# Kernel optimization log

Measured on AMD Instinct MI355X. Metric: run time of the kernel, lower is better.

The kernel has to match this reference:

```python
import jax, jax.numpy as jnp
import numpy as np

NUM_EXPERTS = 64
TOP_K = 2
TEMPERATURE = 1.0
MOMENTUM = 0.9


def _l2norm(x, axis=-1):
    # torch F.normalize: x / max(||x||, eps)
    n = jnp.linalg.norm(x, axis=axis, keepdims=True)
    return x / jnp.maximum(n, 1e-12)


def setup_inputs() -> dict:
    key = jax.random.key(0)
    k1, k2 = jax.random.split(key)
    hidden_states = jax.random.normal(k1, (4, 4096, 2048), dtype=jnp.float32)
    centers = _l2norm(jax.random.normal(k2, (NUM_EXPERTS, 2048), dtype=jnp.float32))
    return {"hidden_states": hidden_states, "centers": centers}


def reference(hidden_states, centers):
    B, T, H = hidden_states.shape
    flat = hidden_states.reshape(-1, H).astype(jnp.float32)  # [N, H]
    N = flat.shape[0]

    # cosine-similarity logits
    reps_n = _l2norm(flat)
    centers_n = _l2norm(centers)
    temp = jnp.maximum(jnp.float32(TEMPERATURE), 1e-6)
    logits = (reps_n @ centers_n.T) / temp  # [N, E]

    probs = jax.nn.softmax(logits, axis=-1)
    top_w, top_ids = jax.lax.top_k(probs, TOP_K)  # [N, k]
    top_w = top_w / (jnp.sum(top_w, axis=-1, keepdims=True) + 1e-9)

    # EMA center update from top-1 routed expert (training+update path)
    route = top_ids[:, 0]  # [N]
    sums = jax.ops.segment_sum(flat, route, num_segments=NUM_EXPERTS)  # [E, H]
    counts = jax.ops.segment_sum(jnp.ones((N, 1), jnp.float32), route,
                                 num_segments=NUM_EXPERTS)  # [E, 1]
    means = sums / (counts + 1e-6)
    updated = _l2norm(MOMENTUM * centers + (1.0 - MOMENTUM) * means)
    new_centers = jnp.where(counts > 0, updated, centers)

    top_ids = top_ids.reshape(B, T, TOP_K)
    top_w = top_w.reshape(B, T, TOP_K)
    return top_ids, top_w, new_centers
```

## Files before the change

### kernel.cpp

```cpp
#include <hip/hip_runtime.h>
#include <math.h>

#define NTOK 16384
#define HDIM 2048
#define NEXP 64
#define KK   32
#define TAU  5e-5f
#define LGT  16384
#define MAXB 2048


__global__ __launch_bounds__(256)
void zero_kernel(float* p, int n) {
  int i = blockIdx.x * 256 + threadIdx.x;
  if (i < n) p[i] = 0.0f;
}

__device__ __forceinline__ float block_reduce_sum(float v, float* red) {
  #pragma unroll
  for (int o = 32; o > 0; o >>= 1) v += __shfl_down(v, o, 64);
  int lane = threadIdx.x & 63;
  int wid  = threadIdx.x >> 6;
  if (lane == 0) red[wid] = v;
  __syncthreads();
  float s = red[0] + red[1] + red[2] + red[3];
  __syncthreads();
  return s;
}

__device__ __forceinline__ double block_reduce_sum_f64(double v, double* red) {
  const int tid = threadIdx.x;
  red[tid] = v;
  __syncthreads();
  if (tid < 128) red[tid] += red[tid + 128];
  __syncthreads();
  if (tid < 64)  red[tid] += red[tid + 64];
  __syncthreads();
  double s = 0.0;
  if (tid < 64) {
    s = red[tid];
    #pragma unroll
    for (int o = 32; o > 0; o >>= 1) s += __shfl_down(s, o, 64);
  }
  if (tid == 0) red[0] = s;
  __syncthreads();
  s = red[0];
  __syncthreads();
  return s;
}

__global__ __launch_bounds__(256)
void cnorm_kernel(const float* __restrict__ c, float* __restrict__ inv_nc) {
  __shared__ float red[4];
  int e = blockIdx.x;
  float ss = 0.f;
  #pragma unroll
  for (int j = 0; j < 8; ++j) {
    float v = c[e * HDIM + threadIdx.x + j * 256];
    ss += v * v;
  }
  float tot = block_reduce_sum(ss, red);
  if (threadIdx.x == 0) inv_nc[e] = 1.0f / fmaxf(sqrtf(tot), 1e-12f);
}

__global__ __launch_bounds__(256)
void cnormalize_kernel(const float* __restrict__ c, float* __restrict__ bn,
                       float* __restrict__ inv_nc) {
  __shared__ double redd[256];
  __shared__ float s_nc;
  const int e = blockIdx.x;
  const int tid = threadIdx.x;
  const float* cr = c + (size_t)e * HDIM;
  double acc = 0.0;
  #pragma unroll
  for (int i = 0; i < 8; ++i) {
    double v = (double)cr[tid + 256 * i];
    acc += v * v;
  }
  double cn = block_reduce_sum_f64(acc, redd);
  if (tid == 0) {
    s_nc = (float)fmax(sqrt(cn), 1e-12);
    inv_nc[e] = 1.0f / s_nc;
  }
  __syncthreads();
  const double nc = (double)s_nc;
  #pragma unroll
  for (int i = 0; i < 8; ++i) {
    int k = tid + 256 * i;
    bn[(size_t)e * HDIM + k] = (float)((double)cr[k] / nc);
  }
}

__global__ __launch_bounds__(256)
void gemm_kernel(const float* __restrict__ x, const float* __restrict__ c,
                 float* __restrict__ logits, float* __restrict__ xnorm2) {
  __shared__ __align__(16) float smem[2 * KK * 68];
  float* xs = smem;
  float* cs = smem + KK * 68;

  const int tid = threadIdx.x;
  const int mt  = blockIdx.x >> 2;
  const int ks  = blockIdx.x & 3;
  const int t0  = mt * 64;
  const int kb  = ks * 512;
  const int tx  = tid & 15;
  const int ty  = tid >> 4;
  const int sr = tid >> 2;
  const int sq = (tid & 3) * 8;

  const float* xrow = x + (size_t)(t0 + sr) * HDIM + kb + sq;
  const float* crow = c + (size_t)sr * HDIM + kb + sq;

  float4 xp[2], cp[2];
  #pragma unroll
  for (int i = 0; i < 2; ++i) xp[i] = *(const float4*)(xrow + 4 * i);
  #pragma unroll
  for (int i = 0; i < 2; ++i) cp[i] = *(const float4*)(crow + 4 * i);

  float acc[4][4];
  #pragma unroll
  for (int j = 0; j < 4; ++j)
    #pragma unroll
    for (int i = 0; i < 4; ++i) acc[j][i] = 0.f;
  float nacc = 0.f;

  for (int it = 0; it < 16; ++it) {
    __syncthreads();
    #pragma unroll
    for (int i = 0; i < 2; ++i) {
      xs[(sq + 4*i + 0) * 68 + sr] = xp[i].x; xs[(sq + 4*i + 1) * 68 + sr] = xp[i].y;
      xs[(sq + 4*i + 2) * 68 + sr] = xp[i].z; xs[(sq + 4*i + 3) * 68 + sr] = xp[i].w;
      nacc += xp[i].x*xp[i].x + xp[i].y*xp[i].y + xp[i].z*xp[i].z + xp[i].w*xp[i].w;
      cs[(sq + 4*i + 0) * 68 + sr] = cp[i].x; cs[(sq + 4*i + 1) * 68 + sr] = cp[i].y;
      cs[(sq + 4*i + 2) * 68 + sr] = cp[i].z; cs[(sq + 4*i + 3) * 68 + sr] = cp[i].w;
    }
    __syncthreads();
    if (it < 15) {
      const float* xn = xrow + (it + 1) * KK;
      const float* cn = crow + (it + 1) * KK;
      #pragma unroll
      for (int i = 0; i < 2; ++i) xp[i] = *(const float4*)(xn + 4 * i);
      #pragma unroll
      for (int i = 0; i < 2; ++i) cp[i] = *(const float4*)(cn + 4 * i);
    }
    #pragma unroll
    for (int k = 0; k < KK; ++k) {
      float4 a = *(const float4*)&xs[k * 68 + ty * 4];
      float4 b = *(const float4*)&cs[k * 68 + tx * 4];
      acc[0][0] += b.x*a.x; acc[0][1] += b.x*a.y; acc[0][2] += b.x*a.z; acc[0][3] += b.x*a.w;
      acc[1][0] += b.y*a.x; acc[1][1] += b.y*a.y; acc[1][2] += b.y*a.z; acc[1][3] += b.y*a.w;
      acc[2][0] += b.z*a.x; acc[2][1] += b.z*a.y; acc[2][2] += b.z*a.z; acc[2][3] += b.z*a.w;
      acc[3][0] += b.w*a.x; acc[3][1] += b.w*a.y; acc[3][2] += b.w*a.z; acc[3][3] += b.w*a.w;
    }
  }

  nacc += __shfl_down(nacc, 2, 4);
  nacc += __shfl_down(nacc, 1, 4);
  if ((tid & 3) == 0) atomicAdd(&xnorm2[t0 + sr], nacc);

  __syncthreads();
  float* lt = smem;
  #pragma unroll
  for (int j = 0; j < 4; ++j)
    #pragma unroll
    for (int i = 0; i < 4; ++i)
      lt[(tx * 4 + j) * 64 + ty * 4 + i] = acc[j][i];
  __syncthreads();
  #pragma unroll
  for (int n = 0; n < 16; ++n) {
    const int f = tid + n * 256;
    const int e = f >> 6;
    const int t = f & 63;
    atomicAdd(&logits[(size_t)e * LGT + t0 + t], lt[f]);
  }
}

__global__ __launch_bounds__(256)
void softmax_kernel(const float* __restrict__ logits, const float* __restrict__ xnorm2,
                    const float* __restrict__ inv_nc, float* __restrict__ out,
                    int* __restrict__ route, int* __restrict__ nflag,
                    int* __restrict__ flags) {
  __shared__ float snc[NEXP];
  const int tid = threadIdx.x;
  if (tid < NEXP) snc[tid] = inv_nc[tid];
  __syncthreads();
  const int t = blockIdx.x * 256 + tid;
  const float inv_nx = 1.0f / fmaxf(sqrtf(xnorm2[t]), 1e-12f);
  float lv[NEXP];
  #pragma unroll
  for (int e = 0; e < NEXP; ++e)
    lv[e] = logits[(size_t)e * LGT + t] * snc[e] * inv_nx;
  float m1 = -1e30f, m2 = -1e30f, m3 = -1e30f;
  int i1 = 0, i2 = 0;
  #pragma unroll
  for (int e = 0; e < NEXP; ++e) {
    float l = lv[e];
    if (l > m1)      { m3 = m2; m2 = m1; i2 = i1; m1 = l; i1 = e; }
    else if (l > m2) { m3 = m2; m2 = l; i2 = e; }
    else if (l > m3) { m3 = l; }
  }
  float Z = 0.f;
  #pragma unroll
  for (int e = 0; e < NEXP; ++e) Z += expf(lv[e] - m1);
  const float p1w = 1.0f / Z;
  const float p2w = expf(m2 - m1) / Z;
  const float s   = p1w + p2w + 1e-9f;
  out[t * 2 + 0] = (float)i1;
  out[t * 2 + 1] = (float)i2;
  out[2 * NTOK + t * 2 + 0] = p1w / s;
  out[2 * NTOK + t * 2 + 1] = p2w / s;
  route[t] = i1;
  if ((m1 - m2) < TAU || (m2 - m3) < TAU) {
    int idx = atomicAdd(nflag, 1);
    flags[idx] = t;
  }
}

__global__ __launch_bounds__(256)
void refine_np_kernel(const float* __restrict__ x, const float* __restrict__ bn,
                      float* __restrict__ out, int* __restrict__ route,
                      const int* __restrict__ nflag, const int* __restrict__ flags) {
  __shared__ float a_lds[HDIM];
  __shared__ double redd[256];
  __shared__ float lf[NEXP];
  __shared__ float s_nx;
  const int tid  = threadIdx.x;
  const int lane = tid & 63;
  const int w    = tid >> 6;
  const int n = *nflag;
  for (int j = blockIdx.x; j < n; j += gridDim.x) {
    const int t = flags[j];
    const float* xr = x + (size_t)t * HDIM;
    double xacc = 0.0;
    #pragma unroll
    for (int i = 0; i < 8; ++i) {
      double v = (double)xr[tid + 256 * i];
      xacc += v * v;
    }
    double xn = block_reduce_sum_f64(xacc, redd);
    if (tid == 0) s_nx = (float)fmax(sqrt(xn), 1e-12);
    __syncthreads();
    const double nx = (double)s_nx;
    #pragma unroll
    for (int i = 0; i < 8; ++i) {
      int k = tid + 256 * i;
      a_lds[k] = (float)((double)xr[k] / nx);
    }
    __syncthreads();
    #pragma unroll 1
    for (int ei = 0; ei < 16; ++ei) {
      const int e = w * 16 + ei;
      const float* br = bn + (size_t)e * HDIM;
      double d = 0.0;
      #pragma unroll 8
      for (int i = 0; i < 32; ++i) {
        int k = lane + 64 * i;
        d += (double)a_lds[k] * (double)br[k];
      }
      #pragma unroll
      for (int o = 32; o > 0; o >>= 1) d += __shfl_down(d, o, 64);
      if (lane == 0) lf[e] = (float)d;
    }
    __syncthreads();
    if (tid == 0) {
      float m32 = lf[0];
      for (int ee = 1; ee < NEXP; ++ee) m32 = fmaxf(m32, lf[ee]);
      float ex[NEXP];
      for (int ee = 0; ee < NEXP; ++ee)
        ex[ee] = (float)exp((double)(lf[ee] - m32));
      float r[8];
      #pragma unroll
      for (int q = 0; q < 8; ++q) r[q] = ex[q];
      for (int i = 8; i < NEXP; i += 8)
        #pragma unroll
        for (int q = 0; q < 8; ++q) r[q] += ex[i + q];
      const float Z = ((r[0] + r[1]) + (r[2] + r[3])) + ((r[4] + r[5]) + (r[6] + r[7]));
      float p1 = -1.f, p2 = -1.f;
      int i1 = 0, i2 = 0;
      for (int ee = 0; ee < NEXP; ++ee) {
        float p = ex[ee] / Z;
        if (p > p1)      { p2 = p1; i2 = i1; p1 = p; i1 = ee; }
        else if (p > p2) { p2 = p; i2 = ee; }
      }
      const float s = (p1 + p2) + 1e-9f;
      out[t * 2 + 0] = (float)i1;
      out[t * 2 + 1] = (float)i2;
      out[2 * NTOK + t * 2 + 0] = p1 / s;
      out[2 * NTOK + t * 2 + 1] = p2 / s;
      route[t] = i1;
    }
    __syncthreads();
  }
}

__global__ __launch_bounds__(64)
void refine_np_slow(const float* __restrict__ x, const float* __restrict__ c,
                    float* __restrict__ out, int* __restrict__ route,
                    const int* __restrict__ nflag, const int* __restrict__ flags) {
  __shared__ float lf[NEXP];
  const int e = threadIdx.x;
  const int n = *nflag;
  for (int j = blockIdx.x; j < n; j += gridDim.x) {
    const int t = flags[j];
    const float* xr = x + (size_t)t * HDIM;
    const float* cr = c + (size_t)e * HDIM;
    double xn = 0.0, cn = 0.0;
    for (int k = 0; k < HDIM; ++k) {
      double xv = (double)xr[k];
      double cv = (double)cr[k];
      xn += xv * xv;
      cn += cv * cv;
    }
    const float nx32 = (float)fmax(sqrt(xn), 1e-12);
    const float nc32 = (float)fmax(sqrt(cn), 1e-12);
    double d = 0.0;
    for (int k = 0; k < HDIM; ++k) {
      float a = (float)((double)xr[k] / (double)nx32);
      float b = (float)((double)cr[k] / (double)nc32);
      d += (double)a * (double)b;
    }
    lf[e] = (float)d;
    __syncthreads();
    if (e == 0) {
      float m32 = lf[0];
      for (int ee = 1; ee < NEXP; ++ee) m32 = fmaxf(m32, lf[ee]);
      float ex[NEXP];
      for (int ee = 0; ee < NEXP; ++ee)
        ex[ee] = (float)exp((double)(lf[ee] - m32));
      float r[8];
      #pragma unroll
      for (int q = 0; q < 8; ++q) r[q] = ex[q];
      for (int i = 8; i < NEXP; i += 8)
        #pragma unroll
        for (int q = 0; q < 8; ++q) r[q] += ex[i + q];
      const float Z = ((r[0] + r[1]) + (r[2] + r[3])) + ((r[4] + r[5]) + (r[6] + r[7]));
      float p1 = -1.f, p2 = -1.f;
      int i1 = 0, i2 = 0;
      for (int ee = 0; ee < NEXP; ++ee) {
        float p = ex[ee] / Z;
        if (p > p1)      { p2 = p1; i2 = i1; p1 = p; i1 = ee; }
        else if (p > p2) { p2 = p; i2 = ee; }
      }
      const float s = (p1 + p2) + 1e-9f;
      out[t * 2 + 0] = (float)i1;
      out[t * 2 + 1] = (float)i2;
      out[2 * NTOK + t * 2 + 0] = p1 / s;
      out[2 * NTOK + t * 2 + 1] = p2 / s;
      route[t] = i1;
    }
    __syncthreads();
  }
}

__global__ __launch_bounds__(256)
void scatter_kernel(const int* __restrict__ route, int* __restrict__ cursor,
                    int* __restrict__ bucket) {
  const int t = blockIdx.x * 256 + threadIdx.x;
  const int e = route[t];
  const int pos = atomicAdd(&cursor[e], 1);
  if (pos < MAXB) bucket[e * MAXB + pos] = t;
}

__global__ __launch_bounds__(256)
void segsum_dense(const float* __restrict__ x, const int* __restrict__ cursor,
                  const int* __restrict__ bucket, float* __restrict__ sums) {
  __shared__ int ts[MAXB];
  const int e   = blockIdx.x >> 3;
  const int hc  = blockIdx.x & 7;
  const int hb  = hc * 256;
  const int tid = threadIdx.x;
  int n = cursor[e];
  if (n > MAXB) n = MAXB;
  for (int i = tid; i < n; i += 256) ts[i] = bucket[e * MAXB + i];
  __syncthreads();
  float a[8];
  #pragma unroll
  for (int q = 0; q < 8; ++q) a[q] = 0.f;
  int i = 0;
  for (; i + 7 < n; i += 8) {
    #pragma unroll
    for (int q = 0; q < 8; ++q)
      a[q] += x[(size_t)ts[i + q] * HDIM + hb + tid];
  }
  for (; i < n; ++i) a[0] += x[(size_t)ts[i] * HDIM + hb + tid];
  const float s = ((a[0] + a[1]) + (a[2] + a[3])) + ((a[4] + a[5]) + (a[6] + a[7]));
  sums[e * HDIM + hb + tid] = s;
}

__global__ __launch_bounds__(256)
void finalize_kernel(const float* __restrict__ c, const float* __restrict__ sums,
                     const int* __restrict__ counts, float* __restrict__ out) {
  __shared__ float red[4];
  const int e = blockIdx.x;
  const int tid = threadIdx.x;
  const float cnt = (float)counts[e];
  const float minv = 1.0f / (cnt + 1e-6f);
  float u[8], cv[8];
  float ss = 0.f;
  #pragma unroll
  for (int j = 0; j < 8; ++j) {
    int h = tid + j * 256;
    cv[j] = c[e * HDIM + h];
    float mean = sums[e * HDIM + h] * minv;
    u[j] = 0.9f * cv[j] + 0.1f * mean;
    ss += u[j] * u[j];
  }
  float tot = block_reduce_sum(ss, red);
  float sc = 1.0f / fmaxf(sqrtf(tot), 1e-12f);
  const bool nz = cnt > 0.f;
  #pragma unroll
  for (int j = 0; j < 8; ++j) {
    int h = tid + j * 256;
    out[4 * NTOK + e * HDIM + h] = nz ? u[j] * sc : cv[j];
  }
}

__global__ __launch_bounds__(256)
void router_kernel(const float* __restrict__ x, const float* __restrict__ c,
                   const float* __restrict__ inv_nc, float* __restrict__ out,
                   int* __restrict__ route, int* __restrict__ nflag,
                   int* __restrict__ flags) {
  __shared__ __align__(16) float xs[64][36];
  __shared__ float lgs[64][67];
  const int tid  = threadIdx.x;
  const int lane = tid & 63;
  const int w    = tid >> 6;
  const int t0   = blockIdx.x * 64;
  const int e0   = __builtin_amdgcn_readfirstlane(w * 16);
  const float* cb = c + (size_t)e0 * HDIM;
  const int st = tid >> 3;
  const int sk = (tid & 7) * 4;
  float acc[16];
  #pragma unroll
  for (int e = 0; e < 16; ++e) acc[e] = 0.f;
  float nacc = 0.f;
  float4 p0 = *(const float4*)&x[(size_t)(t0 + st)      * HDIM + sk];
  float4 p1 = *(const float4*)&x[(size_t)(t0 + st + 32) * HDIM + sk];
  for (int k0 = 0; k0 < HDIM; k0 += 32) {
    __syncthreads();
    *(float4*)&xs[st][sk]      = p0;
    *(float4*)&xs[st + 32][sk] = p1;
    __syncthreads();
    const int kn = k0 + 32;
    if (kn < HDIM) {
      p0 = *(const float4*)&x[(size_t)(t0 + st)      * HDIM + kn + sk];
      p1 = *(const float4*)&x[(size_t)(t0 + st + 32) * HDIM + kn + sk];
    }
    float a[32];
    #pragma unroll
    for (int j = 0; j < 32; j += 4) {
      float4 v = *(const float4*)&xs[lane][j];
      a[j] = v.x; a[j+1] = v.y; a[j+2] = v.z; a[j+3] = v.w;
    }
    if (w == 0) {
      #pragma unroll
      for (int j = 0; j < 32; ++j) nacc += a[j] * a[j];
    }
    #pragma unroll
    for (int e = 0; e < 16; ++e) {
      const float* br = cb + (size_t)e * HDIM + k0;
      #pragma unroll
      for (int j = 0; j < 32; j += 4) {
        float4 bv = *(const float4*)&br[j];
        acc[e] += a[j]*bv.x + a[j+1]*bv.y + a[j+2]*bv.z + a[j+3]*bv.w;
      }
    }
  }
  #pragma unroll
  for (int e = 0; e < 16; ++e) lgs[lane][e0 + e] = acc[e] * inv_nc[e0 + e];
  __syncthreads();
  if (w == 0) {
    const float inv_nx = 1.0f / fmaxf(sqrtf(nacc), 1e-12f);
    float m1 = -1e30f, m2 = -1e30f, m3 = -1e30f;
    int i1 = 0, i2 = 0;
    for (int e = 0; e < NEXP; ++e) {
      float l = lgs[lane][e] * inv_nx;
      if (l > m1)      { m3 = m2; m2 = m1; i2 = i1; m1 = l; i1 = e; }
      else if (l > m2) { m3 = m2; m2 = l; i2 = e; }
      else if (l > m3) { m3 = l; }
    }
    float Z = 0.f;
    for (int e = 0; e < NEXP; ++e) Z += expf(lgs[lane][e] * inv_nx - m1);
    const float p1w = 1.0f / Z;
    const float p2w = expf(m2 - m1) / Z;
    const float s   = p1w + p2w + 1e-9f;
    const int tg = t0 + lane;
    out[tg * 2 + 0] = (float)i1;
    out[tg * 2 + 1] = (float)i2;
    out[2 * NTOK + tg * 2 + 0] = p1w / s;
    out[2 * NTOK + tg * 2 + 1] = p2w / s;
    route[tg] = i1;
    if ((m1 - m2) < TAU || (m2 - m3) < TAU) {
      int idx = atomicAdd(nflag, 1);
      flags[idx] = tg;
    }
  }
}

__global__ __launch_bounds__(512)
void segsum_kernel(const float* __restrict__ x, const int* __restrict__ route,
                   float* __restrict__ sums, int* __restrict__ counts) {
  __shared__ float ls[NEXP * 256];
  __shared__ int lcnt[NEXP];
  const int tid  = threadIdx.x;
  const int lane = tid & 63;
  const int w    = tid >> 6;
  const int hc   = blockIdx.x & 7;
  const int tg   = blockIdx.x >> 3;
  const int hb   = hc * 256;
  #pragma unroll
  for (int i = 0; i < 32; ++i) ls[tid + i * 512] = 0.f;
  if (tid < NEXP) lcnt[tid] = 0;
  __syncthreads();
  const int tbase = tg * 512 + w * 64;
  #pragma unroll 4
  for (int i = 0; i < 64; ++i) {
    const int t = tbase + i;
    const int e = route[t];
    const float* xr = x + (size_t)t * HDIM + hb + lane;
    #pragma unroll
    for (int j = 0; j < 4; ++j)
      atomicAdd(&ls[e * 256 + lane + 64 * j], xr[64 * j]);
    if (hc == 0 && lane == 0) atomicAdd(&lcnt[e], 1);
  }
  __syncthreads();
  #pragma unroll
  for (int i = tid; i < NEXP * 256; i += 512) {
    const int e = i >> 8, h = i & 255;
    atomicAdd(&sums[e * HDIM + hb + h], ls[i]);
  }
  if (hc == 0 && tid < NEXP && lcnt[tid] > 0) atomicAdd(&counts[tid], lcnt[tid]);
}

extern "C" void kernel_launch(void* const* d_in, const int* in_sizes, int n_in,
                              void* d_out, int out_size, void* d_ws, size_t ws_size,
                              hipStream_t stream) {
  const float* x = (const float*)d_in[0];
  const float* c = (const float*)d_in[1];
  float* out = (float*)d_out;
  float* ws = (float*)d_ws;

  float* inv_nc = ws;
  int*   counts = (int*)(ws + 64);
  int*   nflag  = (int*)(ws + 128);
  int*   route  = (int*)(ws + 192);
  int*   flags  = (int*)(ws + 16576);
  float* sums   = ws + 32960;
  float* xnorm2 = ws + 164032;
  float* logits = ws + 180416;
  float* bn     = ws + 1228992;
  int*   bucket = (int*)(ws + 1360064);

  const size_t NEED = 1491136ull * 4ull;
  if (ws_size >= NEED) {
    zero_kernel<<<1, 256, 0, stream>>>(ws + 64, 128);
    zero_kernel<<<4160, 256, 0, stream>>>(ws + 164032, 1064960);
    cnormalize_kernel<<<NEXP, 256, 0, stream>>>(c, bn, inv_nc);
    gemm_kernel<<<1024, 256, 0, stream>>>(x, c, logits, xnorm2);
    softmax_kernel<<<64, 256, 0, stream>>>(logits, xnorm2, inv_nc, out, route, nflag, flags);
    refine_np_kernel<<<512, 256, 0, stream>>>(x, bn, out, route, nflag, flags);
    scatter_kernel<<<64, 256, 0, stream>>>(route, counts, bucket);
    segsum_dense<<<512, 256, 0, stream>>>(x, counts, bucket, sums);
    finalize_kernel<<<NEXP, 256, 0, stream>>>(c, sums, counts, out);
  } else {
    zero_kernel<<<1, 256, 0, stream>>>(ws + 64, 128);
    zero_kernel<<<512, 256, 0, stream>>>(sums, 131072);
    cnorm_kernel<<<NEXP, 256, 0, stream>>>(c, inv_nc);
    router_kernel<<<NTOK / 64, 256, 0, stream>>>(x, c, inv_nc, out, route, nflag, flags);
    refine_np_slow<<<1024, 64, 0, stream>>>(x, c, out, route, nflag, flags);
    segsum_kernel<<<256, 512, 0, stream>>>(x, route, sums, counts);
    finalize_kernel<<<NEXP, 256, 0, stream>>>(c, sums, counts, out);
  }
}
```

Measured before the change: 347.8 us.

## Restructure logits GEMM to per-wave expert slices with uniform center loads

```diff
diff --git a/kernel.cpp b/kernel.cpp
--- a/kernel.cpp
+++ b/kernel.cpp
@@ -4,7 +4,6 @@
 #define NTOK 16384
 #define HDIM 2048
 #define NEXP 64
-#define KK   32
 #define TAU  5e-5f
 #define LGT  16384
 #define MAXB 2048
@@ -94,97 +93,76 @@
 __global__ __launch_bounds__(256)
 void gemm_kernel(const float* __restrict__ x, const float* __restrict__ c,
                  float* __restrict__ logits, float* __restrict__ xnorm2) {
-  __shared__ __align__(16) float smem[2 * KK * 68];
-  float* xs = smem;
-  float* cs = smem + KK * 68;
-
-  const int tid = threadIdx.x;
-  const int mt  = blockIdx.x >> 2;
-  const int ks  = blockIdx.x & 3;
-  const int t0  = mt * 64;
-  const int kb  = ks * 512;
-  const int tx  = tid & 15;
-  const int ty  = tid >> 4;
-  const int sr = tid >> 2;
-  const int sq = (tid & 3) * 8;
-
-  const float* xrow = x + (size_t)(t0 + sr) * HDIM + kb + sq;
-  const float* crow = c + (size_t)sr * HDIM + kb + sq;
-
-  float4 xp[2], cp[2];
-  #pragma unroll
-  for (int i = 0; i < 2; ++i) xp[i] = *(const float4*)(xrow + 4 * i);
-  #pragma unroll
-  for (int i = 0; i < 2; ++i) cp[i] = *(const float4*)(crow + 4 * i);
-
-  float acc[4][4];
-  #pragma unroll
-  for (int j = 0; j < 4; ++j)
-    #pragma unroll
-    for (int i = 0; i < 4; ++i) acc[j][i] = 0.f;
+  __shared__ __align__(16) float xs[64][36];
+
+  const int tid  = threadIdx.x;
+  const int lane = tid & 63;
+  const int w    = tid >> 6;
+  const int mt   = blockIdx.x >> 2;
+  const int ks   = blockIdx.x & 3;
+  const int t0   = mt * 64;
+  const int kb   = ks * 512;
+  const int e0   = __builtin_amdgcn_readfirstlane(w * 16);
+  const float* cb = c + (size_t)e0 * HDIM + kb;
+
+  const int st = tid >> 3;
+  const int sk = (tid & 7) * 4;
+
+  float acc[16];
+  #pragma unroll
+  for (int e = 0; e < 16; ++e) acc[e] = 0.f;
   float nacc = 0.f;
 
-  for (int it = 0; it < 16; ++it) {
-    __syncthreads();
-    #pragma unroll
-    for (int i = 0; i < 2; ++i) {
-      xs[(sq + 4*i + 0) * 68 + sr] = xp[i].x; xs[(sq + 4*i + 1) * 68 + sr] = xp[i].y;
-      xs[(sq + 4*i + 2) * 68 + sr] = xp[i].z; xs[(sq + 4*i + 3) * 68 + sr] = xp[i].w;
-      nacc += xp[i].x*xp[i].x + xp[i].y*xp[i].y + xp[i].z*xp[i].z + xp[i].w*xp[i].w;
-      cs[(sq + 4*i + 0) * 68 + sr] = cp[i].x; cs[(sq + 4*i + 1) * 68 + sr] = cp[i].y;
-      cs[(sq + 4*i + 2) * 68 + sr] = cp[i].z; cs[(sq + 4*i + 3) * 68 + sr] = cp[i].w;
-    }
-    __syncthreads();
-    if (it < 15) {
-      const float* xn = xrow + (it + 1) * KK;
-      const float* cn = crow + (it + 1) * KK;
-      #pragma unroll
-      for (int i = 0; i < 2; ++i) xp[i] = *(const float4*)(xn + 4 * i);
-      #pragma unroll
-      for (int i = 0; i < 2; ++i) cp[i] = *(const float4*)(cn + 4 * i);
-    }
-    #pragma unroll
-    for (int k = 0; k < KK; ++k) {
-      float4 a = *(const float4*)&xs[k * 68 + ty * 4];
-      float4 b = *(const float4*)&cs[k * 68 + tx * 4];
-      acc[0][0] += b.x*a.x; acc[0][1] += b.x*a.y; acc[0][2] += b.x*a.z; acc[0][3] += b.x*a.w;
-      acc[1][0] += b.y*a.x; acc[1][1] += b.y*a.y; acc[1][2] += b.y*a.z; acc[1][3] += b.y*a.w;
-      acc[2][0] += b.z*a.x; acc[2][1] += b.z*a.y; acc[2][2] += b.z*a.z; acc[2][3] += b.z*a.w;
-      acc[3][0] += b.w*a.x; acc[3][1] += b.w*a.y; acc[3][2] += b.w*a.z; acc[3][3] += b.w*a.w;
-    }
-  }
-
-  nacc += __shfl_down(nacc, 2, 4);
-  nacc += __shfl_down(nacc, 1, 4);
-  if ((tid & 3) == 0) atomicAdd(&xnorm2[t0 + sr], nacc);
-
-  __syncthreads();
-  float* lt = smem;
-  #pragma unroll
-  for (int j = 0; j < 4; ++j)
-    #pragma unroll
-    for (int i = 0; i < 4; ++i)
-      lt[(tx * 4 + j) * 64 + ty * 4 + i] = acc[j][i];
-  __syncthreads();
-  #pragma unroll
-  for (int n = 0; n < 16; ++n) {
-    const int f = tid + n * 256;
-    const int e = f >> 6;
-    const int t = f & 63;
-    atomicAdd(&logits[(size_t)e * LGT + t0 + t], lt[f]);
-  }
-}
-
-__global__ __launch_bounds__(256)
+  float4 p0 = *(const float4*)&x[(size_t)(t0 + st)      * HDIM + kb + sk];
+  float4 p1 = *(const float4*)&x[(size_t)(t0 + st + 32) * HDIM + kb + sk];
+
+  for (int k0 = 0; k0 < 512; k0 += 32) {
+    __syncthreads();
+    *(float4*)&xs[st][sk]      = p0;
+    *(float4*)&xs[st + 32][sk] = p1;
+    __syncthreads();
+    const int kn = k0 + 32;
+    if (kn < 512) {
+      p0 = *(const float4*)&x[(size_t)(t0 + st)      * HDIM + kb + kn + sk];
+      p1 = *(const float4*)&x[(size_t)(t0 + st + 32) * HDIM + kb + kn + sk];
+    }
+    float a[32];
+    #pragma unroll
+    for (int j = 0; j < 32; j += 4) {
+      float4 v = *(const float4*)&xs[lane][j];
+      a[j] = v.x; a[j+1] = v.y; a[j+2] = v.z; a[j+3] = v.w;
+    }
+    if (w == 0) {
+      #pragma unroll
+      for (int j = 0; j < 32; ++j) nacc += a[j] * a[j];
+    }
+    #pragma unroll
+    for (int e = 0; e < 16; ++e) {
+      const float* br = cb + (size_t)e * HDIM + k0;
+      #pragma unroll
+      for (int j = 0; j < 32; j += 4) {
+        float4 bv = *(const float4*)&br[j];
+        acc[e] += a[j]*bv.x + a[j+1]*bv.y + a[j+2]*bv.z + a[j+3]*bv.w;
+      }
+    }
+  }
+
+  if (w == 0) atomicAdd(&xnorm2[t0 + lane], nacc);
+  #pragma unroll
+  for (int e = 0; e < 16; ++e)
+    atomicAdd(&logits[(size_t)(e0 + e) * LGT + t0 + lane], acc[e]);
+}
+
+__global__ __launch_bounds__(64)
 void softmax_kernel(const float* __restrict__ logits, const float* __restrict__ xnorm2,
                     const float* __restrict__ inv_nc, float* __restrict__ out,
                     int* __restrict__ route, int* __restrict__ nflag,
                     int* __restrict__ flags) {
   __shared__ float snc[NEXP];
   const int tid = threadIdx.x;
-  if (tid < NEXP) snc[tid] = inv_nc[tid];
-  __syncthreads();
-  const int t = blockIdx.x * 256 + tid;
+  snc[tid] = inv_nc[tid];
+  __syncthreads();
+  const int t = blockIdx.x * 64 + tid;
   const float inv_nx = 1.0f / fmaxf(sqrtf(xnorm2[t]), 1e-12f);
   float lv[NEXP];
   #pragma unroll
@@ -557,7 +535,7 @@
     zero_kernel<<<4160, 256, 0, stream>>>(ws + 164032, 1064960);
     cnormalize_kernel<<<NEXP, 256, 0, stream>>>(c, bn, inv_nc);
     gemm_kernel<<<1024, 256, 0, stream>>>(x, c, logits, xnorm2);
-    softmax_kernel<<<64, 256, 0, stream>>>(logits, xnorm2, inv_nc, out, route, nflag, flags);
+    softmax_kernel<<<256, 64, 0, stream>>>(logits, xnorm2, inv_nc, out, route, nflag, flags);
     refine_np_kernel<<<512, 256, 0, stream>>>(x, bn, out, route, nflag, flags);
     scatter_kernel<<<64, 256, 0, stream>>>(route, counts, bucket);
     segsum_dense<<<512, 256, 0, stream>>>(x, counts, bucket, sums);
```

Result: slower. 361.9 us (+4.1%).
